# Kernel optimization log

Measured on AMD Instinct MI355X. Metric: run time of the kernel, lower is better.

## Reference

```python
import jax, jax.numpy as jnp
import numpy as np

EPS = 1e-5
B, T, D, H = 4096, 256, 36, 64


def setup_inputs() -> dict:
    key = jax.random.key(0)
    ks = jax.random.split(key, 24)
    f32 = jnp.float32
    u = lambda k, shape, s: jax.random.uniform(k, shape, f32, -s, s)
    sH = 1.0 / np.sqrt(H)   # GRUCell / Linear(in=64) init scale
    sD = 1.0 / np.sqrt(D)
    sC = 1.0 / np.sqrt(2 * D)  # combine Linear(72,36)
    return {
        "values": jax.random.normal(ks[0], (B, T, D), f32),
        "masks": (jax.random.uniform(ks[1], (B, T, D)) > 0.2).astype(f32),
        "deltas": jax.random.uniform(ks[2], (B, T, D), f32) * 5.0,
        "label": (jax.random.uniform(ks[3], (B,)) > 0.5).astype(f32),
        "is_train": jnp.ones((B,), f32),
        # GRUCell(108, 64): gate order r, z, n (PyTorch convention)
        "W_ih": u(ks[4], (3 * H, 3 * D), sH),
        "W_hh": u(ks[5], (3 * H, H), sH),
        "b_ih": u(ks[6], (3 * H,), sH),
        "b_hh": u(ks[7], (3 * H,), sH),
        "hist_W": u(ks[8], (1, H), sH),
        "hist_b": u(ks[9], (1,), sH),
        "feat_W": u(ks[10], (D, D), sD),
        "feat_b": u(ks[11], (D,), sD),
        "decay_W": u(ks[12], (D, D), sD),
        "decay_b": u(ks[13], (D,), sD),
        "comb_W": u(ks[14], (D, 2 * D), sC),
        "comb_b": u(ks[15], (D,), sC),
        "out_W": u(ks[16], (1, H), sH),
        "out_b": u(ks[17], (1,), sH),
    }


def reference(values, masks, deltas, label, is_train,
              W_ih, W_hh, b_ih, b_hh, hist_W, hist_b,
              feat_W, feat_b, decay_W, decay_b,
              comb_W, comb_b, out_W, out_b):
    feat_Wm = feat_W * (1.0 - jnp.eye(D, dtype=feat_W.dtype))  # zero diagonal

    def step(carry, xs):
        h, h_sum, il = carry
        value, mask, delta = xs  # each [B, D]
        msum = jnp.sum(mask) + EPS
        value_x = h @ hist_W.T + hist_b                      # [B, 1], broadcasts
        il = il + jnp.sum(jnp.abs(value_x - value) * mask) / msum
        value_c = mask * value + (1.0 - mask) * value_x
        gamma = jnp.exp(-jax.nn.relu(delta @ decay_W.T + decay_b))
        beta = jax.nn.sigmoid(jnp.concatenate([gamma, mask], axis=1) @ comb_W.T + comb_b)
        value_z = value_c @ feat_Wm.T + feat_b
        il = il + jnp.sum(jnp.abs(value_z - value) * mask) / msum
        value_h = value_z * beta + value_x * (1.0 - beta)
        il = il + jnp.sum(jnp.abs(value_h - value) * mask) / msum
        value_c = mask * value + (1.0 - mask) * value_h
        x = jnp.concatenate([value_c, mask, gamma], axis=1)  # [B, 3D]
        gi = x @ W_ih.T + b_ih
        gh = h @ W_hh.T + b_hh
        i_r, i_z, i_n = jnp.split(gi, 3, axis=1)
        h_r, h_z, h_n = jnp.split(gh, 3, axis=1)
        r = jax.nn.sigmoid(i_r + h_r)
        z = jax.nn.sigmoid(i_z + h_z)
        n = jnp.tanh(i_n + r * h_n)
        h_new = (1.0 - z) * n + z * h
        return (h_new, h_sum + h_new, il), value_c

    init = (jnp.zeros((B, H), values.dtype),
            jnp.zeros((B, H), values.dtype),
            jnp.zeros((), values.dtype))
    xs = (values.transpose(1, 0, 2), masks.transpose(1, 0, 2), deltas.transpose(1, 0, 2))
    (h, h_sum, impute_loss), imp = jax.lax.scan(step, init, xs)

    impute_loss = impute_loss / T
    h_sum = h_sum / T
    logits = h_sum @ out_W.T + out_b                          # [B, 1]
    y = label.reshape(-1, 1)
    w = is_train.reshape(-1, 1)
    # binary_cross_entropy_with_logits, reduce=False
    bce = jnp.maximum(logits, 0.0) - logits * y + jnp.log1p(jnp.exp(-jnp.abs(logits)))
    class_loss = jnp.sum(bce * w) / (jnp.sum(w) + EPS)
    loss = class_loss + impute_loss  # alpha = 1.0
    pred = jax.nn.sigmoid(logits)
    impute_values = imp.transpose(1, 0, 2).reshape(B, T * D)  # concat over time on dim 1
    return loss, impute_values, pred
```

## Files before the change

### kernel.cpp

```cpp
#include <hip/hip_runtime.h>
#include <hip/hip_bf16.h>


#define Bsz 4096
#define Tn  256
#define Dn  36
#define ROWS 16
#define EPSf 1e-5f
#define VMST 38

using f32x4 = __attribute__((ext_vector_type(4))) float;
using s8    = __attribute__((ext_vector_type(8))) short;

__device__ __forceinline__ short f2bf(float x) {
  return (short)__bfloat16_as_ushort(__float2bfloat16(x));
}
__device__ __forceinline__ float sigf(float x) { return 1.f / (1.f + __expf(-x)); }
__device__ __forceinline__ float tanhfast(float x) { return 1.f - 2.f / (1.f + __expf(2.f * x)); }
__device__ __forceinline__ int fragoff(int row, int k) {
  return ((k >> 5) << 9) + (((k >> 3) & 3) << 7) + (row << 3) + (k & 7);
}
__device__ __forceinline__ float selq(f32x4 v, int s) {
  float a = (s & 1) ? v[1] : v[0];
  float b = (s & 1) ? v[3] : v[2];
  return (s & 2) ? b : a;
}
#define MFMA __builtin_amdgcn_mfma_f32_16x16x32_bf16

__global__ void msum_k(const float4* __restrict__ masks4, float* __restrict__ rmsum) {
  int t = blockIdx.x;
  float s = 0.f;
  for (int r = threadIdx.x; r < Bsz; r += 256) {
    const float4* mp = masks4 + ((size_t)r * Tn + t) * 9;
    #pragma unroll
    for (int j = 0; j < 9; ++j) { float4 v = mp[j]; s += v.x + v.y + v.z + v.w; }
  }
  __shared__ float red[256];
  red[threadIdx.x] = s;
  __syncthreads();
  for (int k = 128; k > 0; k >>= 1) {
    if (threadIdx.x < k) red[threadIdx.x] += red[threadIdx.x + k];
    __syncthreads();
  }
  if (threadIdx.x == 0) rmsum[t] = 1.f / (red[0] + EPSf);
}

__global__ __launch_bounds__(512) void brits_main(
    const float* __restrict__ values, const float* __restrict__ masks,
    const float* __restrict__ deltas, const float* __restrict__ label,
    const float* __restrict__ is_train,
    const float* __restrict__ W_ih, const float* __restrict__ W_hh,
    const float* __restrict__ b_ih, const float* __restrict__ b_hh,
    const float* __restrict__ hist_W, const float* __restrict__ hist_b,
    const float* __restrict__ feat_W, const float* __restrict__ feat_b,
    const float* __restrict__ decay_W, const float* __restrict__ decay_b,
    const float* __restrict__ comb_W, const float* __restrict__ comb_b,
    const float* __restrict__ out_W, const float* __restrict__ out_b,
    float* __restrict__ out, const float* __restrict__ rmsum,
    float* __restrict__ ws_acc ) {

  __shared__ __align__(16) float2 vm_s[2][ROWS * VMST];
  __shared__ __align__(16) short hbuf[1024];
  __shared__ __align__(16) short dbuf[2][1024];
  __shared__ __align__(16) short mvbuf[2][1024];
  __shared__ __align__(16) short xbuf[2][2048];
  __shared__ float red_s[512];
  __shared__ float red16[16];

  const int tid  = threadIdx.x;
  const int w    = tid >> 6;
  const int lane = tid & 63;
  const int lc   = lane & 15;
  const int r4   = lane >> 4;
  const int row0 = blockIdx.x * ROWS;
  const int k0b  = r4 * 8;
  const int lw8  = lane * 8;

  const bool isG = (w < 4);
  const int  sW  = isG ? 0 : (w - 4);
  const int  dim = 16 * (isG ? w : 0) + lc;
  const int  myrow = 4 * r4 + sW;

  s8 bf[23];
  #pragma unroll
  for (int i = 0; i < 23; ++i) bf[i] = (s8)(short)0;

  if (isG) {
    #pragma unroll
    for (int g = 0; g < 3; ++g) {
      const int n = 64 * g + dim;
      #pragma unroll
      for (int kt = 0; kt < 4; ++kt) {
        s8 f;
        #pragma unroll
        for (int e = 0; e < 8; ++e) {
          int xk = k0b + 32 * kt + e;
          float wv = 0.f;
          if (xk < 72) wv = W_ih[n * 108 + 36 + xk];
          else if (xk < 108) wv = W_ih[n * 108 + xk - 72];
          f[e] = f2bf(wv);
        }
        bf[g * 4 + kt] = f;
      }
      #pragma unroll
      for (int kt = 0; kt < 2; ++kt) {
        s8 f;
        #pragma unroll
        for (int e = 0; e < 8; ++e) f[e] = f2bf(W_hh[n * 64 + k0b + 32 * kt + e]);
        bf[12 + g * 2 + kt] = f;
      }
    }
  } else {
    #pragma unroll
    for (int t3 = 0; t3 < 3; ++t3) {
      const int col = 16 * t3 + lc;
      const bool cok = (col < Dn);
      #pragma unroll
      for (int kt = 0; kt < 2; ++kt) {
        s8 fd, ff;
        #pragma unroll
        for (int e = 0; e < 8; ++e) {
          int k = k0b + 32 * kt + e;
          fd[e] = f2bf((cok && k < Dn) ? decay_W[col * Dn + k] : 0.f);
          ff[e] = f2bf((cok && k < Dn && k != col) ? feat_W[col * Dn + k] : 0.f);
        }
        bf[t3 * 2 + kt] = fd;
        bf[6 + t3 * 2 + kt] = ff;
      }
      #pragma unroll
      for (int kt = 0; kt < 3; ++kt) {
        s8 f;
        #pragma unroll
        for (int e = 0; e < 8; ++e) {
          int xk = k0b + 32 * kt + e;
          float wv = 0.f;
          if (cok) {
            if (xk < 36) wv = comb_W[col * 72 + 36 + xk];
            else if (xk < 72) wv = comb_W[col * 72 + xk - 36];
          }
          f[e] = f2bf(wv);
        }
        bf[14 + t3 * 3 + kt] = f;
      }
    }
    #pragma unroll
    for (int kt = 0; kt < 2; ++kt) {
      s8 f;
      #pragma unroll
      for (int e = 0; e < 8; ++e) f[e] = f2bf(hist_W[k0b + 32 * kt + e]);
      bf[12 + kt] = f;
    }
  }

  float db3[3] = {0,0,0}, fb3[3] = {0,0,0}, cb3[3] = {0,0,0}, wfs3[3] = {0,0,0};
  float br = 0.f, bz = 0.f, bin_ = 0.f, bhn = 0.f, ow = 0.f;
  if (isG) {
    br   = b_ih[dim] + b_hh[dim];
    bz   = b_ih[64 + dim] + b_hh[64 + dim];
    bin_ = b_ih[128 + dim];
    bhn  = b_hh[128 + dim];
    ow   = out_W[dim];
  } else {
    #pragma unroll
    for (int t3 = 0; t3 < 3; ++t3) {
      int col = 16 * t3 + lc;
      if (col < Dn) {
        db3[t3] = decay_b[col]; fb3[t3] = feat_b[col]; cb3[t3] = comb_b[col];
        float s = 0.f;
        for (int k = 0; k < Dn; ++k) if (k != col) s += feat_W[col * Dn + k];
        wfs3[t3] = s;
      }
    }
  }
  const float histb = hist_b[0];
  const int hb = fragoff(0, dim);

  const bool stg = (tid < 144);
  const int srow = tid / 9;
  const int squad = tid - srow * 9;
  const size_t sbase = ((size_t)(row0 + srow) * Tn) * Dn + squad * 4;
  const int sfo = fragoff(srow, squad * 4);
  const int svo = srow * VMST + squad * 4;

  for (int i = tid; i < 1024; i += 512) {
    hbuf[i] = 0; dbuf[0][i] = 0; dbuf[1][i] = 0;
    mvbuf[0][i] = 0; mvbuf[1][i] = 0;
  }
  for (int i = tid; i < 2048; i += 512) { xbuf[0][i] = 0; xbuf[1][i] = 0; }
  __syncthreads();

  float4 pv = {0,0,0,0}, pm = {0,0,0,0}, pd = {0,0,0,0};
  if (stg) {
    float4 v0 = *(const float4*)&values[sbase];
    float4 m0 = *(const float4*)&masks[sbase];
    float4 d0 = *(const float4*)&deltas[sbase];
    *(float4*)&vm_s[0][svo]     = make_float4(v0.x, m0.x, v0.y, m0.y);
    *(float4*)&vm_s[0][svo + 2] = make_float4(v0.z, m0.z, v0.w, m0.w);
    union { short s[4]; uint2 u; } td, tm, tv;
    td.s[0]=f2bf(d0.x); td.s[1]=f2bf(d0.y); td.s[2]=f2bf(d0.z); td.s[3]=f2bf(d0.w);
    tm.s[0]=f2bf(m0.x); tm.s[1]=f2bf(m0.y); tm.s[2]=f2bf(m0.z); tm.s[3]=f2bf(m0.w);
    tv.s[0]=f2bf(m0.x*v0.x); tv.s[1]=f2bf(m0.y*v0.y);
    tv.s[2]=f2bf(m0.z*v0.z); tv.s[3]=f2bf(m0.w*v0.w);
    *(uint2*)&dbuf[0][sfo] = td.u;
    *(uint2*)&xbuf[0][sfo] = tm.u;
    *(uint2*)&mvbuf[0][sfo] = tv.u;
    pv = *(const float4*)&values[sbase + Dn];
    pm = *(const float4*)&masks[sbase + Dn];
    pd = *(const float4*)&deltas[sbase + Dn];
  }
  __syncthreads();

  float bq[3] = {0,0,0}, mvv[3] = {0,0,0}, msv[3] = {0,0,0};
  if (!isG) {
    s8 ad0 = *(const s8*)&dbuf[0][lw8];
    s8 ad1 = *(const s8*)&dbuf[0][512 + lw8];
    s8 am0 = *(const s8*)&xbuf[0][lw8];
    s8 am1 = *(const s8*)&xbuf[0][512 + lw8];
    s8 av0 = *(const s8*)&mvbuf[0][lw8];
    s8 av1 = *(const s8*)&mvbuf[0][512 + lw8];
    f32x4 G0={0,0,0,0}, G1={0,0,0,0}, G2={0,0,0,0};
    f32x4 S0={0,0,0,0}, S1={0,0,0,0}, S2={0,0,0,0};
    f32x4 V0={0,0,0,0}, V1={0,0,0,0}, V2={0,0,0,0};
    G0 = MFMA(ad0, bf[0], G0, 0,0,0); G0 = MFMA(ad1, bf[1], G0, 0,0,0);
    G1 = MFMA(ad0, bf[2], G1, 0,0,0); G1 = MFMA(ad1, bf[3], G1, 0,0,0);
    G2 = MFMA(ad0, bf[4], G2, 0,0,0); G2 = MFMA(ad1, bf[5], G2, 0,0,0);
    S0 = MFMA(am0, bf[6], S0, 0,0,0); S0 = MFMA(am1, bf[7], S0, 0,0,0);
    S1 = MFMA(am0, bf[8], S1, 0,0,0); S1 = MFMA(am1, bf[9], S1, 0,0,0);
    S2 = MFMA(am0, bf[10], S2, 0,0,0); S2 = MFMA(am1, bf[11], S2, 0,0,0);
    V0 = MFMA(av0, bf[6], V0, 0,0,0); V0 = MFMA(av1, bf[7], V0, 0,0,0);
    V1 = MFMA(av0, bf[8], V1, 0,0,0); V1 = MFMA(av1, bf[9], V1, 0,0,0);
    V2 = MFMA(av0, bf[10], V2, 0,0,0); V2 = MFMA(av1, bf[11], V2, 0,0,0);
    #pragma unroll
    for (int t3 = 0; t3 < 3; ++t3) {
      int col = 16 * t3 + lc;
      if (col < Dn) {
        float gm = (t3==0) ? selq(G0,sW) : (t3==1) ? selq(G1,sW) : selq(G2,sW);
        xbuf[0][fragoff(myrow, 36 + col)] = f2bf(__expf(-fmaxf(gm + db3[t3], 0.f)));
      }
      msv[t3] = (t3==0) ? selq(S0,sW) : (t3==1) ? selq(S1,sW) : selq(S2,sW);
      mvv[t3] = (t3==0) ? selq(V0,sW) : (t3==1) ? selq(V1,sW) : selq(V2,sW);
    }
    s8 ac1 = *(const s8*)&xbuf[0][512 + lw8];
    s8 ac2 = *(const s8*)&xbuf[0][1024 + lw8];
    f32x4 B0={0,0,0,0}, B1={0,0,0,0}, B2={0,0,0,0};
    B0 = MFMA(am0, bf[14], B0, 0,0,0); B0 = MFMA(ac1, bf[15], B0, 0,0,0);
    B0 = MFMA(ac2, bf[16], B0, 0,0,0);
    B1 = MFMA(am0, bf[17], B1, 0,0,0); B1 = MFMA(ac1, bf[18], B1, 0,0,0);
    B1 = MFMA(ac2, bf[19], B1, 0,0,0);
    B2 = MFMA(am0, bf[20], B2, 0,0,0); B2 = MFMA(ac1, bf[21], B2, 0,0,0);
    B2 = MFMA(ac2, bf[22], B2, 0,0,0);
    bq[0] = sigf(selq(B0,sW) + cb3[0]);
    bq[1] = sigf(selq(B1,sW) + cb3[1]);
    bq[2] = sigf(selq(B2,sW) + cb3[2]);
  }

  float hreg[4] = {0.f, 0.f, 0.f, 0.f};
  float lacc[4] = {0.f, 0.f, 0.f, 0.f};
  float il = 0.f;
  __syncthreads();

  #pragma unroll 2
  for (int t = 0; t < Tn; ++t) {
    const float srm = rmsum[t];
    const int p = t & 1;
    short* __restrict__ xb  = xbuf[p];
    short* __restrict__ xb2 = xbuf[p ^ 1];
    short* __restrict__ db2 = dbuf[p ^ 1];
    short* __restrict__ mv2 = mvbuf[p ^ 1];
    f32x4 A0 = {0,0,0,0}, A1 = {0,0,0,0}, A2 = {0,0,0,0}, A3 = {0,0,0,0};

    if (isG) {
      s8 ah0 = *(const s8*)&hbuf[lw8];
      s8 ah1 = *(const s8*)&hbuf[512 + lw8];
      A0 = MFMA(ah0, bf[12], A0, 0,0,0); A0 = MFMA(ah1, bf[13], A0, 0,0,0);
      A1 = MFMA(ah0, bf[14], A1, 0,0,0); A1 = MFMA(ah1, bf[15], A1, 0,0,0);
      A3 = MFMA(ah0, bf[16], A3, 0,0,0); A3 = MFMA(ah1, bf[17], A3, 0,0,0);
      s8 ax0 = *(const s8*)&xb[lw8];
      s8 ax1 = *(const s8*)&xb[512 + lw8];
      A0 = MFMA(ax0, bf[0], A0, 0,0,0); A0 = MFMA(ax1, bf[1], A0, 0,0,0);
      A1 = MFMA(ax0, bf[4], A1, 0,0,0); A1 = MFMA(ax1, bf[5], A1, 0,0,0);
      A2 = MFMA(ax0, bf[8], A2, 0,0,0); A2 = MFMA(ax1, bf[9], A2, 0,0,0);
      if (stg && t + 1 < Tn) {
        *(float4*)&vm_s[p ^ 1][svo]     = make_float4(pv.x, pm.x, pv.y, pm.y);
        *(float4*)&vm_s[p ^ 1][svo + 2] = make_float4(pv.z, pm.z, pv.w, pm.w);
        union { short s[4]; uint2 u; } td, tm, tv;
        td.s[0]=f2bf(pd.x); td.s[1]=f2bf(pd.y); td.s[2]=f2bf(pd.z); td.s[3]=f2bf(pd.w);
        tm.s[0]=f2bf(pm.x); tm.s[1]=f2bf(pm.y); tm.s[2]=f2bf(pm.z); tm.s[3]=f2bf(pm.w);
        tv.s[0]=f2bf(pm.x*pv.x); tv.s[1]=f2bf(pm.y*pv.y);
        tv.s[2]=f2bf(pm.z*pv.z); tv.s[3]=f2bf(pm.w*pv.w);
        *(uint2*)&db2[sfo] = td.u;
        *(uint2*)&xb2[sfo] = tm.u;
        *(uint2*)&mv2[sfo] = tv.u;
      }
      if (stg && t + 2 < Tn) {
        size_t o = sbase + (size_t)(t + 2) * Dn;
        pv = *(const float4*)&values[o];
        pm = *(const float4*)&masks[o];
        pd = *(const float4*)&deltas[o];
      }
    } else {
      s8 ah0 = *(const s8*)&hbuf[lw8];
      s8 ah1 = *(const s8*)&hbuf[512 + lw8];
      f32x4 X = {0,0,0,0};
      X = MFMA(ah0, bf[12], X, 0,0,0);
      X = MFMA(ah1, bf[13], X, 0,0,0);
      const float vx = selq(X, sW) + histb;
      #pragma unroll
      for (int t3 = 0; t3 < 3; ++t3) {
        int col = 16 * t3 + lc;
        if (col < Dn) {
          float2 vm = vm_s[p][myrow * VMST + col];
          float vz = vx * (wfs3[t3] - msv[t3]) + mvv[t3] + fb3[t3];
          float vh = vz * bq[t3] + vx * (1.f - bq[t3]);
          float vc2 = vm.y * vm.x + (1.f - vm.y) * vh;
          il += srm * vm.y *
                (fabsf(vx - vm.x) + fabsf(vz - vm.x) + fabsf(vh - vm.x));
          out[1 + ((size_t)(row0 + myrow) * Tn + t) * Dn + col] = vc2;
          xb[fragoff(myrow, 72 + col)] = f2bf(vc2);
        }
      }
    }
    __syncthreads();

    if (isG) {
      s8 ax2 = *(const s8*)&xb[1024 + lw8];
      s8 ax3 = *(const s8*)&xb[1536 + lw8];
      A0 = MFMA(ax2, bf[2],  A0, 0,0,0); A0 = MFMA(ax3, bf[3],  A0, 0,0,0);
      A1 = MFMA(ax2, bf[6],  A1, 0,0,0); A1 = MFMA(ax3, bf[7],  A1, 0,0,0);
      A2 = MFMA(ax2, bf[10], A2, 0,0,0); A2 = MFMA(ax3, bf[11], A2, 0,0,0);
      #pragma unroll
      for (int q = 0; q < 4; ++q) {
        float rg = sigf(A0[q] + br);
        float zg = sigf(A1[q] + bz);
        float ng = tanhfast(A2[q] + bin_ + rg * (A3[q] + bhn));
        float hn = (1.f - zg) * ng + zg * hreg[q];
        hreg[q] = hn;
        lacc[q] += hn * ow;
        hbuf[hb + (r4 * 4 + q) * 8] = f2bf(hn);
      }
    } else if (t + 1 < Tn) {
      s8 ad0 = *(const s8*)&db2[lw8];
      s8 ad1 = *(const s8*)&db2[512 + lw8];
      s8 am0 = *(const s8*)&xb2[lw8];
      s8 am1 = *(const s8*)&xb2[512 + lw8];
      s8 av0 = *(const s8*)&mv2[lw8];
      s8 av1 = *(const s8*)&mv2[512 + lw8];
      f32x4 G0={0,0,0,0}, G1={0,0,0,0}, G2={0,0,0,0};
      f32x4 S0={0,0,0,0}, S1={0,0,0,0}, S2={0,0,0,0};
      f32x4 V0={0,0,0,0}, V1={0,0,0,0}, V2={0,0,0,0};
      G0 = MFMA(ad0, bf[0], G0, 0,0,0); G0 = MFMA(ad1, bf[1], G0, 0,0,0);
      G1 = MFMA(ad0, bf[2], G1, 0,0,0); G1 = MFMA(ad1, bf[3], G1, 0,0,0);
      G2 = MFMA(ad0, bf[4], G2, 0,0,0); G2 = MFMA(ad1, bf[5], G2, 0,0,0);
      S0 = MFMA(am0, bf[6], S0, 0,0,0); S0 = MFMA(am1, bf[7], S0, 0,0,0);
      S1 = MFMA(am0, bf[8], S1, 0,0,0); S1 = MFMA(am1, bf[9], S1, 0,0,0);
      S2 = MFMA(am0, bf[10], S2, 0,0,0); S2 = MFMA(am1, bf[11], S2, 0,0,0);
      V0 = MFMA(av0, bf[6], V0, 0,0,0); V0 = MFMA(av1, bf[7], V0, 0,0,0);
      V1 = MFMA(av0, bf[8], V1, 0,0,0); V1 = MFMA(av1, bf[9], V1, 0,0,0);
      V2 = MFMA(av0, bf[10], V2, 0,0,0); V2 = MFMA(av1, bf[11], V2, 0,0,0);
      #pragma unroll
      for (int t3 = 0; t3 < 3; ++t3) {
        int col = 16 * t3 + lc;
        if (col < Dn) {
          float gm = (t3==0) ? selq(G0,sW) : (t3==1) ? selq(G1,sW) : selq(G2,sW);
          xb2[fragoff(myrow, 36 + col)] = f2bf(__expf(-fmaxf(gm + db3[t3], 0.f)));
        }
        msv[t3] = (t3==0) ? selq(S0,sW) : (t3==1) ? selq(S1,sW) : selq(S2,sW);
        mvv[t3] = (t3==0) ? selq(V0,sW) : (t3==1) ? selq(V1,sW) : selq(V2,sW);
      }
      s8 ac1 = *(const s8*)&xb2[512 + lw8];
      s8 ac2 = *(const s8*)&xb2[1024 + lw8];
      f32x4 B0={0,0,0,0}, B1={0,0,0,0}, B2={0,0,0,0};
      B0 = MFMA(am0, bf[14], B0, 0,0,0); B0 = MFMA(ac1, bf[15], B0, 0,0,0);
      B0 = MFMA(ac2, bf[16], B0, 0,0,0);
      B1 = MFMA(am0, bf[17], B1, 0,0,0); B1 = MFMA(ac1, bf[18], B1, 0,0,0);
      B1 = MFMA(ac2, bf[19], B1, 0,0,0);
      B2 = MFMA(am0, bf[20], B2, 0,0,0); B2 = MFMA(ac1, bf[21], B2, 0,0,0);
      B2 = MFMA(ac2, bf[22], B2, 0,0,0);
      bq[0] = sigf(selq(B0,sW) + cb3[0]);
      bq[1] = sigf(selq(B1,sW) + cb3[1]);
      bq[2] = sigf(selq(B2,sW) + cb3[2]);
    }
    __syncthreads();
  }

  red_s[tid] = il;
  __syncthreads();
  for (int k = 256; k > 0; k >>= 1) {
    if (tid < k) red_s[tid] += red_s[tid + k];
    __syncthreads();
  }
  if (tid == 0) atomicAdd(&ws_acc[0], red_s[0]);
  if (tid < 16) red16[tid] = 0.f;
  __syncthreads();
  if (isG) {
    #pragma unroll
    for (int q = 0; q < 4; ++q) atomicAdd(&red16[r4 * 4 + q], lacc[q]);
  }
  __syncthreads();

  if (tid < ROWS) {
    float lg = red16[tid] / (float)Tn + out_b[0];
    int rg = row0 + tid;
    float pred = sigf(lg);
    out[1 + (size_t)Bsz * Tn * Dn + rg] = pred;
    float y = label[rg], wt = is_train[rg];
    float bce = fmaxf(lg, 0.f) - lg * y + log1pf(__expf(-fabsf(lg)));
    atomicAdd(&ws_acc[1], bce * wt);
    atomicAdd(&ws_acc[2], wt);
  }
}

__global__ void fin_k(const float* __restrict__ ws, float* __restrict__ out) {
  out[0] = ws[1] / (ws[2] + EPSf) + ws[0] / (float)Tn;
}

extern "C" void kernel_launch(void* const* d_in, const int* in_sizes, int n_in,
                              void* d_out, int out_size, void* d_ws, size_t ws_size,
                              hipStream_t stream) {
  const float* values   = (const float*)d_in[0];
  const float* masks    = (const float*)d_in[1];
  const float* deltas   = (const float*)d_in[2];
  const float* label    = (const float*)d_in[3];
  const float* is_train = (const float*)d_in[4];
  const float* W_ih     = (const float*)d_in[5];
  const float* W_hh     = (const float*)d_in[6];
  const float* b_ih     = (const float*)d_in[7];
  const float* b_hh     = (const float*)d_in[8];
  const float* hist_W   = (const float*)d_in[9];
  const float* hist_b   = (const float*)d_in[10];
  const float* feat_W   = (const float*)d_in[11];
  const float* feat_b   = (const float*)d_in[12];
  const float* decay_W  = (const float*)d_in[13];
  const float* decay_b  = (const float*)d_in[14];
  const float* comb_W   = (const float*)d_in[15];
  const float* comb_b   = (const float*)d_in[16];
  const float* out_W    = (const float*)d_in[17];
  const float* out_b    = (const float*)d_in[18];

  float* ws = (float*)d_ws;
  float* rmsum = ws + 4;
  float* out = (float*)d_out;

  hipMemsetAsync(d_ws, 0, 16, stream);
  msum_k<<<Tn, 256, 0, stream>>>((const float4*)masks, rmsum);
  brits_main<<<Bsz / ROWS, 512, 0, stream>>>(
      values, masks, deltas, label, is_train, W_ih, W_hh, b_ih, b_hh,
      hist_W, hist_b, feat_W, feat_b, decay_W, decay_b, comb_W, comb_b,
      out_W, out_b, out, rmsum, ws);
  fin_k<<<1, 1, 0, stream>>>(ws, out);
}
```

Before: 426.2 us.

## Move imputed-value stores and global prefetch to GRU warps, read back from bf16 LDS

The per-element global store of imputed values moves off the imputation warps. The GRU warps now write them one step later, reading the bf16 copy held in the LDS fragment buffer. This emits bf16-rounded values instead of full fp32, which costs precision. Staging is spread across GRU-warp lanes, and the next-step global loads move after the barrier. The rmsum load is hoisted one step ahead, and the out_W multiply is taken out of the per-step accumulation.

```diff
diff --git a/kernel.cpp b/kernel.cpp
--- a/kernel.cpp
+++ b/kernel.cpp
@@ -175,12 +175,14 @@
   const float histb = hist_b[0];
   const int hb = fragoff(0, dim);
 
-  const bool stg = (tid < 144);
-  const int srow = tid / 9;
-  const int squad = tid - srow * 9;
+  const bool stg = isG && (lane < 36);
+  const int slot = w * 36 + lane;
+  const int srow = slot / 9;
+  const int squad = slot - srow * 9;
   const size_t sbase = ((size_t)(row0 + srow) * Tn) * Dn + squad * 4;
   const int sfo = fragoff(srow, squad * 4);
   const int svo = srow * VMST + squad * 4;
+  const int vfo = fragoff(srow, 72 + squad * 4);
 
   for (int i = tid; i < 1024; i += 512) {
     hbuf[i] = 0; dbuf[0][i] = 0; dbuf[1][i] = 0;
@@ -257,11 +259,11 @@
   float hreg[4] = {0.f, 0.f, 0.f, 0.f};
   float lacc[4] = {0.f, 0.f, 0.f, 0.f};
   float il = 0.f;
+  float srmv = rmsum[0];
   __syncthreads();
 
   #pragma unroll 2
   for (int t = 0; t < Tn; ++t) {
-    const float srm = rmsum[t];
     const int p = t & 1;
     short* __restrict__ xb  = xbuf[p];
     short* __restrict__ xb2 = xbuf[p ^ 1];
@@ -292,12 +294,6 @@
         *(uint2*)&xb2[sfo] = tm.u;
         *(uint2*)&mv2[sfo] = tv.u;
       }
-      if (stg && t + 2 < Tn) {
-        size_t o = sbase + (size_t)(t + 2) * Dn;
-        pv = *(const float4*)&values[o];
-        pm = *(const float4*)&masks[o];
-        pd = *(const float4*)&deltas[o];
-      }
     } else {
       s8 ah0 = *(const s8*)&hbuf[lw8];
       s8 ah1 = *(const s8*)&hbuf[512 + lw8];
@@ -313,9 +309,8 @@
           float vz = vx * (wfs3[t3] - msv[t3]) + mvv[t3] + fb3[t3];
           float vh = vz * bq[t3] + vx * (1.f - bq[t3]);
           float vc2 = vm.y * vm.x + (1.f - vm.y) * vh;
-          il += srm * vm.y *
+          il += srmv * vm.y *
                 (fabsf(vx - vm.x) + fabsf(vz - vm.x) + fabsf(vh - vm.x));
-          out[1 + ((size_t)(row0 + myrow) * Tn + t) * Dn + col] = vc2;
           xb[fragoff(myrow, 72 + col)] = f2bf(vc2);
         }
       }
@@ -325,6 +320,20 @@
     if (isG) {
       s8 ax2 = *(const s8*)&xb[1024 + lw8];
       s8 ax3 = *(const s8*)&xb[1536 + lw8];
+      if (stg && t > 0) {
+        uint2 pk = *(const uint2*)&xb2[vfo];
+        size_t ob = 1 + ((size_t)(row0 + srow) * Tn + (t - 1)) * Dn + squad * 4;
+        out[ob + 0] = __uint_as_float(pk.x << 16);
+        out[ob + 1] = __uint_as_float(pk.x & 0xFFFF0000u);
+        out[ob + 2] = __uint_as_float(pk.y << 16);
+        out[ob + 3] = __uint_as_float(pk.y & 0xFFFF0000u);
+      }
+      if (stg && t + 2 < Tn) {
+        size_t o = sbase + (size_t)(t + 2) * Dn;
+        pv = *(const float4*)&values[o];
+        pm = *(const float4*)&masks[o];
+        pd = *(const float4*)&deltas[o];
+      }
       A0 = MFMA(ax2, bf[2],  A0, 0,0,0); A0 = MFMA(ax3, bf[3],  A0, 0,0,0);
       A1 = MFMA(ax2, bf[6],  A1, 0,0,0); A1 = MFMA(ax3, bf[7],  A1, 0,0,0);
       A2 = MFMA(ax2, bf[10], A2, 0,0,0); A2 = MFMA(ax3, bf[11], A2, 0,0,0);
@@ -335,10 +344,11 @@
         float ng = tanhfast(A2[q] + bin_ + rg * (A3[q] + bhn));
         float hn = (1.f - zg) * ng + zg * hreg[q];
         hreg[q] = hn;
-        lacc[q] += hn * ow;
+        lacc[q] += hn;
         hbuf[hb + (r4 * 4 + q) * 8] = f2bf(hn);
       }
     } else if (t + 1 < Tn) {
+      srmv = rmsum[t + 1];
       s8 ad0 = *(const s8*)&db2[lw8];
       s8 ad1 = *(const s8*)&db2[512 + lw8];
       s8 am0 = *(const s8*)&xb2[lw8];
@@ -383,6 +393,14 @@
     __syncthreads();
   }
 
+  if (stg) {
+    uint2 pk = *(const uint2*)&xbuf[1][vfo];
+    size_t ob = 1 + ((size_t)(row0 + srow) * Tn + (Tn - 1)) * Dn + squad * 4;
+    out[ob + 0] = __uint_as_float(pk.x << 16);
+    out[ob + 1] = __uint_as_float(pk.x & 0xFFFF0000u);
+    out[ob + 2] = __uint_as_float(pk.y << 16);
+    out[ob + 3] = __uint_as_float(pk.y & 0xFFFF0000u);
+  }
   red_s[tid] = il;
   __syncthreads();
   for (int k = 256; k > 0; k >>= 1) {
@@ -394,7 +412,7 @@
   __syncthreads();
   if (isG) {
     #pragma unroll
-    for (int q = 0; q < 4; ++q) atomicAdd(&red16[r4 * 4 + q], lacc[q]);
+    for (int q = 0; q < 4; ++q) atomicAdd(&red16[r4 * 4 + q], lacc[q] * ow);
   }
   __syncthreads();
 
```

After: 535.2 us. 25.6% more time.

## Move input staging to compute waves with register prefetch, drop vm_s LDS buffer

Applied to the files above, without the earlier changes.

Input loading for values, masks and deltas moves from the first 144 threads of the GRU waves to the four non-GRU waves. Each of those waves loads its own row's columns two steps ahead into registers and writes the bf16 fragments itself, which removes the float2 vm_s shared buffer and its LDS reads. The global store of imputed values is deferred into the second phase so the GRU waves no longer issue loads on the critical path. The trade-off is scalar per-column loads in place of float4 loads, which may coalesce less well, plus extra register pressure on the non-GRU waves.

```diff
diff --git a/kernel.cpp b/kernel.cpp
--- a/kernel.cpp
+++ b/kernel.cpp
@@ -7,7 +7,6 @@
 #define Dn  36
 #define ROWS 16
 #define EPSf 1e-5f
-#define VMST 38
 
 using f32x4 = __attribute__((ext_vector_type(4))) float;
 using s8    = __attribute__((ext_vector_type(8))) short;
@@ -59,7 +58,6 @@
     float* __restrict__ out, const float* __restrict__ rmsum,
     float* __restrict__ ws_acc ) {
 
-  __shared__ __align__(16) float2 vm_s[2][ROWS * VMST];
   __shared__ __align__(16) short hbuf[1024];
   __shared__ __align__(16) short dbuf[2][1024];
   __shared__ __align__(16) short mvbuf[2][1024];
@@ -175,12 +173,16 @@
   const float histb = hist_b[0];
   const int hb = fragoff(0, dim);
 
-  const bool stg = (tid < 144);
-  const int srow = tid / 9;
-  const int squad = tid - srow * 9;
-  const size_t sbase = ((size_t)(row0 + srow) * Tn) * Dn + squad * 4;
-  const int sfo = fragoff(srow, squad * 4);
-  const int svo = srow * VMST + squad * 4;
+  const int cc[3] = {lc, 16 + lc, 32 + lc};
+  int foM[3], vfo3[3];
+  #pragma unroll
+  for (int t3 = 0; t3 < 3; ++t3) {
+    int col = cc[t3] < Dn ? cc[t3] : 0;
+    foM[t3]  = fragoff(myrow, col);
+    vfo3[t3] = fragoff(myrow, 72 + col);
+  }
+  const size_t inbase = (size_t)(row0 + myrow) * Tn * Dn;
+  const size_t outbase = 1 + inbase;
 
   for (int i = tid; i < 1024; i += 512) {
     hbuf[i] = 0; dbuf[0][i] = 0; dbuf[1][i] = 0;
@@ -189,35 +191,18 @@
   for (int i = tid; i < 2048; i += 512) { xbuf[0][i] = 0; xbuf[1][i] = 0; }
   __syncthreads();
 
-  float4 pv = {0,0,0,0}, pm = {0,0,0,0}, pd = {0,0,0,0};
-  if (stg) {
-    float4 v0 = *(const float4*)&values[sbase];
-    float4 m0 = *(const float4*)&masks[sbase];
-    float4 d0 = *(const float4*)&deltas[sbase];
-    *(float4*)&vm_s[0][svo]     = make_float4(v0.x, m0.x, v0.y, m0.y);
-    *(float4*)&vm_s[0][svo + 2] = make_float4(v0.z, m0.z, v0.w, m0.w);
-    union { short s[4]; uint2 u; } td, tm, tv;
-    td.s[0]=f2bf(d0.x); td.s[1]=f2bf(d0.y); td.s[2]=f2bf(d0.z); td.s[3]=f2bf(d0.w);
-    tm.s[0]=f2bf(m0.x); tm.s[1]=f2bf(m0.y); tm.s[2]=f2bf(m0.z); tm.s[3]=f2bf(m0.w);
-    tv.s[0]=f2bf(m0.x*v0.x); tv.s[1]=f2bf(m0.y*v0.y);
-    tv.s[2]=f2bf(m0.z*v0.z); tv.s[3]=f2bf(m0.w*v0.w);
-    *(uint2*)&dbuf[0][sfo] = td.u;
-    *(uint2*)&xbuf[0][sfo] = tm.u;
-    *(uint2*)&mvbuf[0][sfo] = tv.u;
-    pv = *(const float4*)&values[sbase + Dn];
-    pm = *(const float4*)&masks[sbase + Dn];
-    pd = *(const float4*)&deltas[sbase + Dn];
-  }
-  __syncthreads();
-
+  float cvv[3] = {0,0,0}, cvm[3] = {0,0,0};
+  float nvv[3] = {0,0,0}, nvm[3] = {0,0,0};
+  float vc2f[3] = {0,0,0};
   float bq[3] = {0,0,0}, mvv[3] = {0,0,0}, msv[3] = {0,0,0};
-  if (!isG) {
-    s8 ad0 = *(const s8*)&dbuf[0][lw8];
-    s8 ad1 = *(const s8*)&dbuf[0][512 + lw8];
-    s8 am0 = *(const s8*)&xbuf[0][lw8];
-    s8 am1 = *(const s8*)&xbuf[0][512 + lw8];
-    s8 av0 = *(const s8*)&mvbuf[0][lw8];
-    s8 av1 = *(const s8*)&mvbuf[0][512 + lw8];
+
+  auto precomp = [&](const short* db_, short* xb_, const short* mv_) {
+    s8 ad0 = *(const s8*)&db_[lw8];
+    s8 ad1 = *(const s8*)&db_[512 + lw8];
+    s8 am0 = *(const s8*)&xb_[lw8];
+    s8 am1 = *(const s8*)&xb_[512 + lw8];
+    s8 av0 = *(const s8*)&mv_[lw8];
+    s8 av1 = *(const s8*)&mv_[512 + lw8];
     f32x4 G0={0,0,0,0}, G1={0,0,0,0}, G2={0,0,0,0};
     f32x4 S0={0,0,0,0}, S1={0,0,0,0}, S2={0,0,0,0};
     f32x4 V0={0,0,0,0}, V1={0,0,0,0}, V2={0,0,0,0};
@@ -235,13 +220,13 @@
       int col = 16 * t3 + lc;
       if (col < Dn) {
         float gm = (t3==0) ? selq(G0,sW) : (t3==1) ? selq(G1,sW) : selq(G2,sW);
-        xbuf[0][fragoff(myrow, 36 + col)] = f2bf(__expf(-fmaxf(gm + db3[t3], 0.f)));
+        xb_[fragoff(myrow, 36 + col)] = f2bf(__expf(-fmaxf(gm + db3[t3], 0.f)));
       }
       msv[t3] = (t3==0) ? selq(S0,sW) : (t3==1) ? selq(S1,sW) : selq(S2,sW);
       mvv[t3] = (t3==0) ? selq(V0,sW) : (t3==1) ? selq(V1,sW) : selq(V2,sW);
     }
-    s8 ac1 = *(const s8*)&xbuf[0][512 + lw8];
-    s8 ac2 = *(const s8*)&xbuf[0][1024 + lw8];
+    s8 ac1 = *(const s8*)&xb_[512 + lw8];
+    s8 ac2 = *(const s8*)&xb_[1024 + lw8];
     f32x4 B0={0,0,0,0}, B1={0,0,0,0}, B2={0,0,0,0};
     B0 = MFMA(am0, bf[14], B0, 0,0,0); B0 = MFMA(ac1, bf[15], B0, 0,0,0);
     B0 = MFMA(ac2, bf[16], B0, 0,0,0);
@@ -252,16 +237,37 @@
     bq[0] = sigf(selq(B0,sW) + cb3[0]);
     bq[1] = sigf(selq(B1,sW) + cb3[1]);
     bq[2] = sigf(selq(B2,sW) + cb3[2]);
-  }
+  };
+
+  if (!isG) {
+    #pragma unroll
+    for (int t3 = 0; t3 < 3; ++t3) {
+      if (cc[t3] < Dn) {
+        int col = cc[t3];
+        cvv[t3] = values[inbase + col]; cvm[t3] = masks[inbase + col];
+        float d0 = deltas[inbase + col];
+        dbuf[0][foM[t3]]  = f2bf(d0);
+        xbuf[0][foM[t3]]  = f2bf(cvm[t3]);
+        mvbuf[0][foM[t3]] = f2bf(cvm[t3] * cvv[t3]);
+        nvv[t3] = values[inbase + Dn + col]; nvm[t3] = masks[inbase + Dn + col];
+        float d1 = deltas[inbase + Dn + col];
+        dbuf[1][foM[t3]]  = f2bf(d1);
+        xbuf[1][foM[t3]]  = f2bf(nvm[t3]);
+        mvbuf[1][foM[t3]] = f2bf(nvm[t3] * nvv[t3]);
+      }
+    }
+  }
+  __syncthreads();
+  if (!isG) precomp(dbuf[0], xbuf[0], mvbuf[0]);
 
   float hreg[4] = {0.f, 0.f, 0.f, 0.f};
   float lacc[4] = {0.f, 0.f, 0.f, 0.f};
   float il = 0.f;
+  float srmv = rmsum[0];
   __syncthreads();
 
   #pragma unroll 2
   for (int t = 0; t < Tn; ++t) {
-    const float srm = rmsum[t];
     const int p = t & 1;
     short* __restrict__ xb  = xbuf[p];
     short* __restrict__ xb2 = xbuf[p ^ 1];
@@ -280,24 +286,6 @@
       A0 = MFMA(ax0, bf[0], A0, 0,0,0); A0 = MFMA(ax1, bf[1], A0, 0,0,0);
       A1 = MFMA(ax0, bf[4], A1, 0,0,0); A1 = MFMA(ax1, bf[5], A1, 0,0,0);
       A2 = MFMA(ax0, bf[8], A2, 0,0,0); A2 = MFMA(ax1, bf[9], A2, 0,0,0);
-      if (stg && t + 1 < Tn) {
-        *(float4*)&vm_s[p ^ 1][svo]     = make_float4(pv.x, pm.x, pv.y, pm.y);
-        *(float4*)&vm_s[p ^ 1][svo + 2] = make_float4(pv.z, pm.z, pv.w, pm.w);
-        union { short s[4]; uint2 u; } td, tm, tv;
-        td.s[0]=f2bf(pd.x); td.s[1]=f2bf(pd.y); td.s[2]=f2bf(pd.z); td.s[3]=f2bf(pd.w);
-        tm.s[0]=f2bf(pm.x); tm.s[1]=f2bf(pm.y); tm.s[2]=f2bf(pm.z); tm.s[3]=f2bf(pm.w);
-        tv.s[0]=f2bf(pm.x*pv.x); tv.s[1]=f2bf(pm.y*pv.y);
-        tv.s[2]=f2bf(pm.z*pv.z); tv.s[3]=f2bf(pm.w*pv.w);
-        *(uint2*)&db2[sfo] = td.u;
-        *(uint2*)&xb2[sfo] = tm.u;
-        *(uint2*)&mv2[sfo] = tv.u;
-      }
-      if (stg && t + 2 < Tn) {
-        size_t o = sbase + (size_t)(t + 2) * Dn;
-        pv = *(const float4*)&values[o];
-        pm = *(const float4*)&masks[o];
-        pd = *(const float4*)&deltas[o];
-      }
     } else {
       s8 ah0 = *(const s8*)&hbuf[lw8];
       s8 ah1 = *(const s8*)&hbuf[512 + lw8];
@@ -307,16 +295,14 @@
       const float vx = selq(X, sW) + histb;
       #pragma unroll
       for (int t3 = 0; t3 < 3; ++t3) {
-        int col = 16 * t3 + lc;
-        if (col < Dn) {
-          float2 vm = vm_s[p][myrow * VMST + col];
+        if (cc[t3] < Dn) {
+          float vv = cvv[t3], mm = cvm[t3];
           float vz = vx * (wfs3[t3] - msv[t3]) + mvv[t3] + fb3[t3];
           float vh = vz * bq[t3] + vx * (1.f - bq[t3]);
-          float vc2 = vm.y * vm.x + (1.f - vm.y) * vh;
-          il += srm * vm.y *
-                (fabsf(vx - vm.x) + fabsf(vz - vm.x) + fabsf(vh - vm.x));
-          out[1 + ((size_t)(row0 + myrow) * Tn + t) * Dn + col] = vc2;
-          xb[fragoff(myrow, 72 + col)] = f2bf(vc2);
+          vc2f[t3] = mm * vv + (1.f - mm) * vh;
+          il += srmv * mm *
+                (fabsf(vx - vv) + fabsf(vz - vv) + fabsf(vh - vv));
+          xb[vfo3[t3]] = f2bf(vc2f[t3]);
         }
       }
     }
@@ -339,50 +325,52 @@
         hbuf[hb + (r4 * 4 + q) * 8] = f2bf(hn);
       }
     } else if (t + 1 < Tn) {
-      s8 ad0 = *(const s8*)&db2[lw8];
-      s8 ad1 = *(const s8*)&db2[512 + lw8];
-      s8 am0 = *(const s8*)&xb2[lw8];
-      s8 am1 = *(const s8*)&xb2[512 + lw8];
-      s8 av0 = *(const s8*)&mv2[lw8];
-      s8 av1 = *(const s8*)&mv2[512 + lw8];
-      f32x4 G0={0,0,0,0}, G1={0,0,0,0}, G2={0,0,0,0};
-      f32x4 S0={0,0,0,0}, S1={0,0,0,0}, S2={0,0,0,0};
-      f32x4 V0={0,0,0,0}, V1={0,0,0,0}, V2={0,0,0,0};
-      G0 = MFMA(ad0, bf[0], G0, 0,0,0); G0 = MFMA(ad1, bf[1], G0, 0,0,0);
-      G1 = MFMA(ad0, bf[2], G1, 0,0,0); G1 = MFMA(ad1, bf[3], G1, 0,0,0);
-      G2 = MFMA(ad0, bf[4], G2, 0,0,0); G2 = MFMA(ad1, bf[5], G2, 0,0,0);
-      S0 = MFMA(am0, bf[6], S0, 0,0,0); S0 = MFMA(am1, bf[7], S0, 0,0,0);
-      S1 = MFMA(am0, bf[8], S1, 0,0,0); S1 = MFMA(am1, bf[9], S1, 0,0,0);
-      S2 = MFMA(am0, bf[10], S2, 0,0,0); S2 = MFMA(am1, bf[11], S2, 0,0,0);
-      V0 = MFMA(av0, bf[6], V0, 0,0,0); V0 = MFMA(av1, bf[7], V0, 0,0,0);
-      V1 = MFMA(av0, bf[8], V1, 0,0,0); V1 = MFMA(av1, bf[9], V1, 0,0,0);
-      V2 = MFMA(av0, bf[10], V2, 0,0,0); V2 = MFMA(av1, bf[11], V2, 0,0,0);
+      srmv = rmsum[t + 1];
+      {
+        size_t ob = outbase + (size_t)t * Dn;
+        out[ob + cc[0]] = vc2f[0];
+        out[ob + cc[1]] = vc2f[1];
+        if (cc[2] < Dn) out[ob + cc[2]] = vc2f[2];
+      }
+      float lv[3] = {0,0,0}, lm[3] = {0,0,0}, ldl[3] = {0,0,0};
+      const bool ld2 = (t + 2 < Tn);
+      if (ld2) {
+        size_t ib = inbase + (size_t)(t + 2) * Dn;
+        #pragma unroll
+        for (int t3 = 0; t3 < 3; ++t3) {
+          if (cc[t3] < Dn) {
+            lv[t3] = values[ib + cc[t3]];
+            lm[t3] = masks[ib + cc[t3]];
+            ldl[t3] = deltas[ib + cc[t3]];
+          }
+        }
+      }
+      precomp(db2, xb2, mv2);
+      if (ld2) {
+        #pragma unroll
+        for (int t3 = 0; t3 < 3; ++t3) {
+          if (cc[t3] < Dn) {
+            dbuf[p][foM[t3]]  = f2bf(ldl[t3]);
+            xbuf[p][foM[t3]]  = f2bf(lm[t3]);
+            mvbuf[p][foM[t3]] = f2bf(lm[t3] * lv[t3]);
+          }
+        }
+      }
       #pragma unroll
       for (int t3 = 0; t3 < 3; ++t3) {
-        int col = 16 * t3 + lc;
-        if (col < Dn) {
-          float gm = (t3==0) ? selq(G0,sW) : (t3==1) ? selq(G1,sW) : selq(G2,sW);
-          xb2[fragoff(myrow, 36 + col)] = f2bf(__expf(-fmaxf(gm + db3[t3], 0.f)));
-        }
-        msv[t3] = (t3==0) ? selq(S0,sW) : (t3==1) ? selq(S1,sW) : selq(S2,sW);
-        mvv[t3] = (t3==0) ? selq(V0,sW) : (t3==1) ? selq(V1,sW) : selq(V2,sW);
-      }
-      s8 ac1 = *(const s8*)&xb2[512 + lw8];
-      s8 ac2 = *(const s8*)&xb2[1024 + lw8];
-      f32x4 B0={0,0,0,0}, B1={0,0,0,0}, B2={0,0,0,0};
-      B0 = MFMA(am0, bf[14], B0, 0,0,0); B0 = MFMA(ac1, bf[15], B0, 0,0,0);
-      B0 = MFMA(ac2, bf[16], B0, 0,0,0);
-      B1 = MFMA(am0, bf[17], B1, 0,0,0); B1 = MFMA(ac1, bf[18], B1, 0,0,0);
-      B1 = MFMA(ac2, bf[19], B1, 0,0,0);
-      B2 = MFMA(am0, bf[20], B2, 0,0,0); B2 = MFMA(ac1, bf[21], B2, 0,0,0);
-      B2 = MFMA(ac2, bf[22], B2, 0,0,0);
-      bq[0] = sigf(selq(B0,sW) + cb3[0]);
-      bq[1] = sigf(selq(B1,sW) + cb3[1]);
-      bq[2] = sigf(selq(B2,sW) + cb3[2]);
+        cvv[t3] = nvv[t3]; cvm[t3] = nvm[t3];
+        nvv[t3] = lv[t3];  nvm[t3] = lm[t3];
+      }
     }
     __syncthreads();
   }
 
+  if (!isG) {
+    size_t ob = outbase + (size_t)(Tn - 1) * Dn;
+    out[ob + cc[0]] = vc2f[0];
+    out[ob + cc[1]] = vc2f[1];
+    if (cc[2] < Dn) out[ob + cc[2]] = vc2f[2];
+  }
   red_s[tid] = il;
   __syncthreads();
   for (int k = 256; k > 0; k >>= 1) {
```

Result: slower. 527.9 us (+23.9%).
